# Optimization experiments

Hardware: AMD Instinct MI355X
Metric: run time of the kernel (lower is better)

## Reference

```python
import jax, jax.numpy as jnp
import numpy as np
import math

D_MODEL = 128
N_HEAD = 8
D_K = D_MODEL // N_HEAD
NEG_INF = -1e30


def setup_inputs() -> dict:
    key = jax.random.key(0)
    ks = jax.random.split(key, 8)
    B, N, D = 4, 2048, D_MODEL
    s = 1.0 / math.sqrt(D)
    x = jax.random.normal(ks[0], (B, D, N), dtype=jnp.float32)
    mask = jnp.ones((B, N), dtype=jnp.float32)
    Wq = jax.random.normal(ks[1], (D, D), dtype=jnp.float32) * s
    Wk = jax.random.normal(ks[2], (D, D), dtype=jnp.float32) * s
    Wv = jax.random.normal(ks[3], (D, D), dtype=jnp.float32) * s
    Wfc = jax.random.normal(ks[4], (D, D), dtype=jnp.float32) * s
    z = jnp.zeros((D,), dtype=jnp.float32)
    return {"x": x, "mask": mask, "Wq": Wq, "bq": z, "Wk": Wk, "bk": z,
            "Wv": Wv, "bv": z, "Wfc": Wfc, "bfc": z}


def reference(x, mask, Wq, bq, Wk, bk, Wv, bv, Wfc, bfc):
    # x: [B, D, N], mask: [B, N]
    B, D, N = x.shape
    xt = jnp.swapaxes(x, 1, 2)  # [B, N, D]
    q = (xt @ Wq.T + bq).reshape(B, N, N_HEAD, D_K)
    k = (xt @ Wk.T + bk).reshape(B, N, N_HEAD, D_K)
    v = (xt @ Wv.T + bv).reshape(B, N, N_HEAD, D_K)
    # scores: [B, H, Nq, Nk]; NOTE: original scales by sqrt(d_model), not sqrt(d_k)
    scores = jnp.einsum('bnhd,bmhd->bhnm', q, k) / jnp.sqrt(jnp.float32(D))
    # multiplicative mask_logits over the key dimension
    m = mask[:, None, None, :]  # [B, 1, 1, Nk]
    scores = scores * m + (1.0 - m) * NEG_INF
    atten = jax.nn.softmax(scores, axis=-1)  # dropout is identity (p=0 / eval)
    out = jnp.einsum('bhnm,bmhd->bnhd', atten, v).reshape(B, N, D)
    out = out @ Wfc.T + bfc
    return jnp.swapaxes(out, 1, 2)  # [B, D, N]
```

## Files before the change

### kernel.cpp

```cpp
#include <hip/hip_runtime.h>
#include <stdint.h>

#define BSZ  4
#define NSEQ 2048
#define DM   128
#define NH   8
#define DK   16
#define LOG2E 1.4426950408889634f

typedef __bf16          bf16x8v __attribute__((ext_vector_type(8)));
typedef float           f32x4   __attribute__((ext_vector_type(4)));
typedef float           f32x16  __attribute__((ext_vector_type(16)));
typedef unsigned short  u16x8   __attribute__((ext_vector_type(8)));
typedef unsigned short  u16x4   __attribute__((ext_vector_type(4)));
typedef unsigned int    u32x2   __attribute__((ext_vector_type(2)));

__device__ __forceinline__ unsigned short f2bf(float f) {
    unsigned u = __float_as_uint(f);
    u = (u + 0x7fffu + ((u >> 16) & 1u)) >> 16;
    return (unsigned short)u;
}

__device__ __forceinline__ unsigned int pack2bf(float a, float b) {
#if __has_builtin(__builtin_amdgcn_cvt_pk_bf16_f32)
    typedef __bf16 bf16x2 __attribute__((ext_vector_type(2)));
    bf16x2 v = __builtin_amdgcn_cvt_pk_bf16_f32(a, b);
    return __builtin_bit_cast(unsigned int, v);
#else
    return (unsigned)f2bf(a) | ((unsigned)f2bf(b) << 16);
#endif
}

__device__ __forceinline__ float exp2_(float x) {
#if __has_builtin(__builtin_amdgcn_exp2f)
    return __builtin_amdgcn_exp2f(x);
#else
    return exp2f(x);
#endif
}

__device__ __forceinline__ f32x4 mfma16(u16x8 a, u16x8 b, f32x4 c) {
    return __builtin_amdgcn_mfma_f32_16x16x32_bf16(
        __builtin_bit_cast(bf16x8v, a), __builtin_bit_cast(bf16x8v, b), c, 0, 0, 0);
}
__device__ __forceinline__ f32x16 mfma32(u16x8 a, u16x8 b, f32x16 c) {
    return __builtin_amdgcn_mfma_f32_32x32x16_bf16(
        __builtin_bit_cast(bf16x8v, a), __builtin_bit_cast(bf16x8v, b), c, 0, 0, 0);
}

__global__ __launch_bounds__(256) void k_conv(
    const float* __restrict__ Wq, const float* __restrict__ Wk,
    const float* __restrict__ Wv, const float* __restrict__ Wfc,
    const float* __restrict__ bq, const float* __restrict__ mask,
    unsigned short* __restrict__ WqB, unsigned short* __restrict__ WkB,
    unsigned short* __restrict__ WvB, unsigned short* __restrict__ WfcB,
    float* __restrict__ bqs, float* __restrict__ mbias)
{
    const int t = blockIdx.x * 256 + threadIdx.x;
    const float s = 0.08838834764831845f;
    WqB[t]  = f2bf(Wq[t] * s);
    WkB[t]  = f2bf(Wk[t]);
    WvB[t]  = f2bf(Wv[t]);
    WfcB[t] = f2bf(Wfc[t]);
    if (t < DM) bqs[t] = bq[t] * s;
    if (t < BSZ * NSEQ) mbias[t] = (1.0f - mask[t]) * (-1e30f);
}

__global__ __launch_bounds__(192) void k_qkv(
    const float* __restrict__ x,
    const unsigned short* __restrict__ WqB, const float* __restrict__ bqs,
    const unsigned short* __restrict__ WkB, const float* __restrict__ bk,
    const unsigned short* __restrict__ WvB, const float* __restrict__ bv,
    unsigned short* __restrict__ Q, unsigned short* __restrict__ Kb,
    unsigned short* __restrict__ Vt)
{
    const int lane = threadIdx.x & 63;
    const int mat  = threadIdx.x >> 6;
    const int c    = lane & 15;
    const int quad = lane >> 4;
    const int b    = blockIdx.x >> 7;
    const int n0   = (blockIdx.x & 127) << 4;

    u16x8 xf[4];
#pragma unroll
    for (int kk = 0; kk < 4; ++kk) {
        u16x8 u;
#pragma unroll
        for (int j = 0; j < 8; ++j)
            u[j] = f2bf(x[(b * DM + kk * 32 + quad * 8 + j) * NSEQ + n0 + c]);
        xf[kk] = u;
    }

    const unsigned short* W    = (mat == 0) ? WqB : (mat == 1) ? WkB : WvB;
    const float*          bias = (mat == 0) ? bqs : (mat == 1) ? bk  : bv;

    for (int t = 0; t < 8; ++t) {
        f32x4 acc = {0.f, 0.f, 0.f, 0.f};
#pragma unroll
        for (int kk = 0; kk < 4; ++kk)
            acc = mfma16(*reinterpret_cast<const u16x8*>(
                             W + (t * 16 + c) * DM + kk * 32 + quad * 8),
                         xf[kk], acc);
        if (mat == 2) {
#pragma unroll
            for (int r = 0; r < 4; ++r)
                Vt[((b * NH + t) * DK + quad * 4 + r) * NSEQ + n0 + c] =
                    f2bf(acc[r] + bias[t * 16 + quad * 4 + r]);
        } else {
            u16x4 pk;
#pragma unroll
            for (int r = 0; r < 4; ++r)
                pk[r] = f2bf(acc[r] + bias[t * 16 + quad * 4 + r]);
            *reinterpret_cast<u16x4*>(
                (mat == 0 ? Q : Kb) + ((size_t)(b * NH + t) * NSEQ + n0 + c) * DK +
                quad * 4) = pk;
        }
    }
}

__global__ __launch_bounds__(256, 4) void k_attn(
    const unsigned short* __restrict__ Q,
    const unsigned short* __restrict__ Kb,
    const unsigned short* __restrict__ Vt,
    const float* __restrict__ mbias,
    unsigned short* __restrict__ AO)
{
    __shared__ __align__(16) char smem[19456];
    const int lane = threadIdx.x & 63;
    const int w    = threadIdx.x >> 6;
    const int q32  = lane & 31;
    const int hi   = lane >> 5;
    const int c    = lane & 15;
    const int quad = lane >> 4;

    const int qt   = blockIdx.x * 2 + (w >> 1);
    const int half = w & 1;
    const int b    = qt >> 9;
    const int h    = (qt >> 6) & 7;
    const int n0   = (qt & 63) << 5;
    const int bh   = b * NH + h;

    const u16x8 uq = *reinterpret_cast<const u16x8*>(
        Q + ((size_t)bh * NSEQ + n0 + q32) * DK + 8 * hi);

    const unsigned short* Kp = Kb + (size_t)bh * NSEQ * DK + 8 * hi;
    const unsigned short* Vp = Vt + ((size_t)bh * DK + c) * NSEQ + 8 * quad;
    const float*          mb = mbias + b * NSEQ + 4 * hi;

    char* pbase = smem + w * 2560;
    char* wrow  = pbase + q32 * 80 + 8 * hi;
    const u16x8* rp0 = reinterpret_cast<const u16x8*>(pbase + c * 80 + 16 * quad);
    const u16x8* rp1 = reinterpret_cast<const u16x8*>(pbase + (c + 16) * 80 + 16 * quad);

    float m_run = -1e30f, l_run = 0.f;
    f32x4 o0 = {0.f, 0.f, 0.f, 0.f}, o1 = {0.f, 0.f, 0.f, 0.f};
    const f32x16 z16 = {};

    const int kvbase = half * (NSEQ / 2);
    for (int it = 0; it < 32; ++it) {
        const int kv0 = kvbase + it * 32;
        const u16x8 uk = *reinterpret_cast<const u16x8*>(Kp + (size_t)(kv0 + q32) * DK);
        f32x16 S = mfma32(uk, uq, z16);

        const f32x4 b0 = *reinterpret_cast<const f32x4*>(mb + kv0);
        const f32x4 b1 = *reinterpret_cast<const f32x4*>(mb + kv0 + 8);
        const f32x4 b2 = *reinterpret_cast<const f32x4*>(mb + kv0 + 16);
        const f32x4 b3 = *reinterpret_cast<const f32x4*>(mb + kv0 + 24);
#pragma unroll
        for (int r = 0; r < 4; ++r) {
            S[r]      += b0[r];
            S[4 + r]  += b1[r];
            S[8 + r]  += b2[r];
            S[12 + r] += b3[r];
        }

        float t8[8];
#pragma unroll
        for (int i = 0; i < 8; ++i) t8[i] = fmaxf(S[i], S[i + 8]);
#pragma unroll
        for (int i = 0; i < 4; ++i) t8[i] = fmaxf(t8[i], t8[i + 4]);
        float mx = fmaxf(fmaxf(t8[0], t8[1]), fmaxf(t8[2], t8[3]));
        mx = fmaxf(mx, __shfl_xor(mx, 32, 64));

        const float mn    = fmaxf(m_run, mx);
        const float mnL   = mn * LOG2E;
        const float alpha = exp2_(fmaf(m_run, LOG2E, -mnL));

        float p[16];
#pragma unroll
        for (int i = 0; i < 16; ++i) p[i] = exp2_(fmaf(S[i], LOG2E, -mnL));
        float s8[8];
#pragma unroll
        for (int i = 0; i < 8; ++i) s8[i] = p[i] + p[i + 8];
#pragma unroll
        for (int i = 0; i < 4; ++i) s8[i] = s8[i] + s8[i + 4];
        float ps = (s8[0] + s8[1]) + (s8[2] + s8[3]);
        ps += __shfl_xor(ps, 32, 64);
        l_run = fmaf(l_run, alpha, ps);
        m_run = mn;

        const float a0 = __shfl(alpha, c, 64);
        const float a1 = __shfl(alpha, c + 16, 64);
#pragma unroll
        for (int r = 0; r < 4; ++r) { o0[r] *= a0; o1[r] *= a1; }

        unsigned int pk[8];
#pragma unroll
        for (int s = 0; s < 8; ++s) pk[s] = pack2bf(p[2 * s], p[2 * s + 1]);
#pragma unroll
        for (int g = 0; g < 4; ++g) {
            u32x2 dv = {pk[2 * g], pk[2 * g + 1]};
            *reinterpret_cast<u32x2*>(wrow + 16 * g) = dv;
        }

        const u16x8 up0 = *rp0;
        const u16x8 up1 = *rp1;
        const u16x8 uv  = *reinterpret_cast<const u16x8*>(Vp + kv0);
        o0 = mfma16(uv, up0, o0);
        o1 = mfma16(uv, up1, o1);
    }

    float* stm = reinterpret_cast<float*>(smem + 10240) + w * 64;
    stm[q32]      = m_run;
    stm[32 + q32] = l_run;
    f32x4* ox = reinterpret_cast<f32x4*>(smem + 11264 + w * 2048);
    ox[lane * 2]     = o0;
    ox[lane * 2 + 1] = o1;
    __syncthreads();

    const int pw = w ^ 1;
    const float* stp = reinterpret_cast<const float*>(smem + 10240) + pw * 64;
    const float m2 = stp[q32];
    const float l2 = stp[32 + q32];
    const float mn   = fmaxf(m_run, m2);
    const float f1   = exp2_((m_run - mn) * LOG2E);
    const float f2   = exp2_((m2 - mn) * LOG2E);
    const float inv  = 1.0f / (l_run * f1 + l2 * f2);
    const float s1   = f1 * inv, s2 = f2 * inv;

    const f32x4* oxp = reinterpret_cast<const f32x4*>(smem + 11264 + pw * 2048);
    const f32x4 po0 = oxp[lane * 2];
    const f32x4 po1 = oxp[lane * 2 + 1];

    const float s1a = __shfl(s1, c, 64),      s2a = __shfl(s2, c, 64);
    const float s1b = __shfl(s1, c + 16, 64), s2b = __shfl(s2, c + 16, 64);

    if (half == 0) {
        u16x4 r0, r1;
#pragma unroll
        for (int r = 0; r < 4; ++r) {
            r0[r] = f2bf(o0[r] * s1a + po0[r] * s2a);
            r1[r] = f2bf(o1[r] * s1b + po1[r] * s2b);
        }
        *reinterpret_cast<u16x4*>(
            AO + ((size_t)(b * NSEQ) + n0 + c) * DM + h * DK + quad * 4) = r0;
        *reinterpret_cast<u16x4*>(
            AO + ((size_t)(b * NSEQ) + n0 + 16 + c) * DM + h * DK + quad * 4) = r1;
    }
}

__global__ __launch_bounds__(256) void k_fc(
    const unsigned short* __restrict__ AO,
    const unsigned short* __restrict__ WfcB, const float* __restrict__ bfc,
    float* __restrict__ out)
{
    const int lane = threadIdx.x & 63;
    const int w    = threadIdx.x >> 6;
    const int c    = lane & 15;
    const int quad = lane >> 4;
    const int b    = blockIdx.x >> 7;
    const int n0   = (blockIdx.x & 127) << 4;

    u16x8 af[4];
#pragma unroll
    for (int kk = 0; kk < 4; ++kk)
        af[kk] = *reinterpret_cast<const u16x8*>(
            AO + ((size_t)(b * NSEQ) + n0 + c) * DM + kk * 32 + quad * 8);

#pragma unroll
    for (int tt = 0; tt < 2; ++tt) {
        const int t = w * 2 + tt;
        f32x4 acc = {0.f, 0.f, 0.f, 0.f};
#pragma unroll
        for (int kk = 0; kk < 4; ++kk)
            acc = mfma16(*reinterpret_cast<const u16x8*>(
                             WfcB + (t * 16 + c) * DM + kk * 32 + quad * 8),
                         af[kk], acc);
#pragma unroll
        for (int r = 0; r < 4; ++r)
            out[(size_t)(b * DM + t * 16 + quad * 4 + r) * NSEQ + n0 + c] =
                acc[r] + bfc[t * 16 + quad * 4 + r];
    }
}

extern "C" void kernel_launch(void* const* d_in, const int* in_sizes, int n_in,
                              void* d_out, int out_size, void* d_ws, size_t ws_size,
                              hipStream_t stream)
{
    const float* x    = (const float*)d_in[0];
    const float* mask = (const float*)d_in[1];
    const float* Wq   = (const float*)d_in[2];
    const float* bq   = (const float*)d_in[3];
    const float* Wk   = (const float*)d_in[4];
    const float* bk   = (const float*)d_in[5];
    const float* Wv   = (const float*)d_in[6];
    const float* bv   = (const float*)d_in[7];
    const float* Wfc  = (const float*)d_in[8];
    const float* bfc  = (const float*)d_in[9];
    float* out = (float*)d_out;

    const size_t QKV_ELEMS = (size_t)BSZ * NH * NSEQ * DK;
    unsigned short* Q    = (unsigned short*)d_ws;
    unsigned short* Kb   = Q + QKV_ELEMS;
    unsigned short* Vt   = Kb + QKV_ELEMS;
    unsigned short* AO   = Vt + QKV_ELEMS;
    unsigned short* WqB  = AO + QKV_ELEMS;
    unsigned short* WkB  = WqB + DM * DM;
    unsigned short* WvB  = WkB + DM * DM;
    unsigned short* WfcB = WvB + DM * DM;
    float* bqs   = (float*)(WfcB + DM * DM);
    float* mbias = bqs + DM;

    k_conv<<<64, 256, 0, stream>>>(Wq, Wk, Wv, Wfc, bq, mask,
                                   WqB, WkB, WvB, WfcB, bqs, mbias);
    k_qkv<<<512, 192, 0, stream>>>(x, WqB, bqs, WkB, bk, WvB, bv, Q, Kb, Vt);
    k_attn<<<1024, 256, 0, stream>>>(Q, Kb, Vt, mbias, AO);
    k_fc<<<512, 256, 0, stream>>>(AO, WfcB, bfc, out);
}
```

Baseline: 136.7 us.

## Split attention KV across four waves, fold log2e into scale, double grids

Each attention block now handles one 32-query tile, and its four waves each cover a quarter of the KV sequence. Each wave processes 64 keys per iteration, and the four partial results are merged in shared memory through a cooperative reduction. The log2e factor is folded into the Q weight scale and the mask bias, which removes the per-element FMAs before exp2. The QKV and FC kernels are split across twice as many blocks to raise parallelism. The cost is larger shared memory use and more blocks with less work each, which adds launch and tail overhead.

```diff
diff --git a/kernel.cpp b/kernel.cpp
--- a/kernel.cpp
+++ b/kernel.cpp
@@ -7,6 +7,7 @@
 #define NH   8
 #define DK   16
 #define LOG2E 1.4426950408889634f
+#define SCALE_QL 0.1275156338341935f
 
 typedef __bf16          bf16x8v __attribute__((ext_vector_type(8)));
 typedef float           f32x4   __attribute__((ext_vector_type(4)));
@@ -57,13 +58,12 @@
     float* __restrict__ bqs, float* __restrict__ mbias)
 {
     const int t = blockIdx.x * 256 + threadIdx.x;
-    const float s = 0.08838834764831845f;
-    WqB[t]  = f2bf(Wq[t] * s);
+    WqB[t]  = f2bf(Wq[t] * SCALE_QL);
     WkB[t]  = f2bf(Wk[t]);
     WvB[t]  = f2bf(Wv[t]);
     WfcB[t] = f2bf(Wfc[t]);
-    if (t < DM) bqs[t] = bq[t] * s;
-    if (t < BSZ * NSEQ) mbias[t] = (1.0f - mask[t]) * (-1e30f);
+    if (t < DM) bqs[t] = bq[t] * SCALE_QL;
+    if (t < BSZ * NSEQ) mbias[t] = (1.0f - mask[t]) * (-1e30f * LOG2E);
 }
 
 __global__ __launch_bounds__(192) void k_qkv(
@@ -78,8 +78,9 @@
     const int mat  = threadIdx.x >> 6;
     const int c    = lane & 15;
     const int quad = lane >> 4;
-    const int b    = blockIdx.x >> 7;
-    const int n0   = (blockIdx.x & 127) << 4;
+    const int b    = blockIdx.x >> 8;
+    const int n0   = ((blockIdx.x >> 1) & 127) << 4;
+    const int th   = blockIdx.x & 1;
 
     u16x8 xf[4];
 #pragma unroll
@@ -94,7 +95,9 @@
     const unsigned short* W    = (mat == 0) ? WqB : (mat == 1) ? WkB : WvB;
     const float*          bias = (mat == 0) ? bqs : (mat == 1) ? bk  : bv;
 
-    for (int t = 0; t < 8; ++t) {
+#pragma unroll
+    for (int tt = 0; tt < 4; ++tt) {
+        const int t = th * 4 + tt;
         f32x4 acc = {0.f, 0.f, 0.f, 0.f};
 #pragma unroll
         for (int kk = 0; kk < 4; ++kk)
@@ -122,79 +125,84 @@
     const unsigned short* __restrict__ Q,
     const unsigned short* __restrict__ Kb,
     const unsigned short* __restrict__ Vt,
-    const float* __restrict__ mbias,
+    const float* __restrict__ mb2,
     unsigned short* __restrict__ AO)
 {
-    __shared__ __align__(16) char smem[19456];
-    const int lane = threadIdx.x & 63;
-    const int w    = threadIdx.x >> 6;
+    __shared__ __align__(16) char smem[28672];
+    const int tid  = threadIdx.x;
+    const int lane = tid & 63;
+    const int w    = tid >> 6;
     const int q32  = lane & 31;
     const int hi   = lane >> 5;
     const int c    = lane & 15;
     const int quad = lane >> 4;
 
-    const int qt   = blockIdx.x * 2 + (w >> 1);
-    const int half = w & 1;
-    const int b    = qt >> 9;
-    const int h    = (qt >> 6) & 7;
-    const int n0   = (qt & 63) << 5;
-    const int bh   = b * NH + h;
+    const int b  = blockIdx.x >> 9;
+    const int h  = (blockIdx.x >> 6) & 7;
+    const int n0 = (blockIdx.x & 63) << 5;
+    const int bh = b * NH + h;
 
     const u16x8 uq = *reinterpret_cast<const u16x8*>(
         Q + ((size_t)bh * NSEQ + n0 + q32) * DK + 8 * hi);
 
     const unsigned short* Kp = Kb + (size_t)bh * NSEQ * DK + 8 * hi;
     const unsigned short* Vp = Vt + ((size_t)bh * DK + c) * NSEQ + 8 * quad;
-    const float*          mb = mbias + b * NSEQ + 4 * hi;
-
-    char* pbase = smem + w * 2560;
-    char* wrow  = pbase + q32 * 80 + 8 * hi;
-    const u16x8* rp0 = reinterpret_cast<const u16x8*>(pbase + c * 80 + 16 * quad);
-    const u16x8* rp1 = reinterpret_cast<const u16x8*>(pbase + (c + 16) * 80 + 16 * quad);
+    const float*          mb = mb2 + b * NSEQ + 4 * hi;
+
+    char* pbase = smem + w * 4352;
+    char* wrow  = pbase + q32 * 136 + 8 * hi;
+    const char* rrow0 = pbase + c * 136 + 16 * quad;
+    const char* rrow1 = pbase + (c + 16) * 136 + 16 * quad;
 
     float m_run = -1e30f, l_run = 0.f;
     f32x4 o0 = {0.f, 0.f, 0.f, 0.f}, o1 = {0.f, 0.f, 0.f, 0.f};
     const f32x16 z16 = {};
-
-    const int kvbase = half * (NSEQ / 2);
-    for (int it = 0; it < 32; ++it) {
-        const int kv0 = kvbase + it * 32;
-        const u16x8 uk = *reinterpret_cast<const u16x8*>(Kp + (size_t)(kv0 + q32) * DK);
-        f32x16 S = mfma32(uk, uq, z16);
-
-        const f32x4 b0 = *reinterpret_cast<const f32x4*>(mb + kv0);
-        const f32x4 b1 = *reinterpret_cast<const f32x4*>(mb + kv0 + 8);
-        const f32x4 b2 = *reinterpret_cast<const f32x4*>(mb + kv0 + 16);
-        const f32x4 b3 = *reinterpret_cast<const f32x4*>(mb + kv0 + 24);
-#pragma unroll
-        for (int r = 0; r < 4; ++r) {
-            S[r]      += b0[r];
-            S[4 + r]  += b1[r];
-            S[8 + r]  += b2[r];
-            S[12 + r] += b3[r];
-        }
-
-        float t8[8];
-#pragma unroll
-        for (int i = 0; i < 8; ++i) t8[i] = fmaxf(S[i], S[i + 8]);
-#pragma unroll
-        for (int i = 0; i < 4; ++i) t8[i] = fmaxf(t8[i], t8[i + 4]);
-        float mx = fmaxf(fmaxf(t8[0], t8[1]), fmaxf(t8[2], t8[3]));
+    const int kvb = w * (NSEQ / 4);
+
+    for (int it = 0; it < 8; ++it) {
+        const int kv0 = kvb + it * 64;
+        const u16x8 uk0 = *reinterpret_cast<const u16x8*>(Kp + (size_t)(kv0 + q32) * DK);
+        const u16x8 uk1 = *reinterpret_cast<const u16x8*>(Kp + (size_t)(kv0 + 32 + q32) * DK);
+        f32x16 S0 = mfma32(uk0, uq, z16);
+        f32x16 S1 = mfma32(uk1, uq, z16);
+
+#pragma unroll
+        for (int g = 0; g < 4; ++g) {
+            const f32x4 bg0 = *reinterpret_cast<const f32x4*>(mb + kv0 + 8 * g);
+            const f32x4 bg1 = *reinterpret_cast<const f32x4*>(mb + kv0 + 32 + 8 * g);
+#pragma unroll
+            for (int r = 0; r < 4; ++r) {
+                S0[4 * g + r] += bg0[r];
+                S1[4 * g + r] += bg1[r];
+            }
+        }
+
+        float t16[16];
+#pragma unroll
+        for (int i = 0; i < 16; ++i) t16[i] = fmaxf(S0[i], S1[i]);
+#pragma unroll
+        for (int i = 0; i < 8; ++i) t16[i] = fmaxf(t16[i], t16[i + 8]);
+#pragma unroll
+        for (int i = 0; i < 4; ++i) t16[i] = fmaxf(t16[i], t16[i + 4]);
+        float mx = fmaxf(fmaxf(t16[0], t16[1]), fmaxf(t16[2], t16[3]));
         mx = fmaxf(mx, __shfl_xor(mx, 32, 64));
 
         const float mn    = fmaxf(m_run, mx);
-        const float mnL   = mn * LOG2E;
-        const float alpha = exp2_(fmaf(m_run, LOG2E, -mnL));
-
-        float p[16];
-#pragma unroll
-        for (int i = 0; i < 16; ++i) p[i] = exp2_(fmaf(S[i], LOG2E, -mnL));
-        float s8[8];
-#pragma unroll
-        for (int i = 0; i < 8; ++i) s8[i] = p[i] + p[i + 8];
-#pragma unroll
-        for (int i = 0; i < 4; ++i) s8[i] = s8[i] + s8[i + 4];
-        float ps = (s8[0] + s8[1]) + (s8[2] + s8[3]);
+        const float alpha = exp2_(m_run - mn);
+
+#pragma unroll
+        for (int i = 0; i < 16; ++i) {
+            S0[i] = exp2_(S0[i] - mn);
+            S1[i] = exp2_(S1[i] - mn);
+        }
+        float s16[16];
+#pragma unroll
+        for (int i = 0; i < 16; ++i) s16[i] = S0[i] + S1[i];
+#pragma unroll
+        for (int i = 0; i < 8; ++i) s16[i] += s16[i + 8];
+#pragma unroll
+        for (int i = 0; i < 4; ++i) s16[i] += s16[i + 4];
+        float ps = (s16[0] + s16[1]) + (s16[2] + s16[3]);
         ps += __shfl_xor(ps, 32, 64);
         l_run = fmaf(l_run, alpha, ps);
         m_run = mn;
@@ -204,59 +212,48 @@
 #pragma unroll
         for (int r = 0; r < 4; ++r) { o0[r] *= a0; o1[r] *= a1; }
 
-        unsigned int pk[8];
-#pragma unroll
-        for (int s = 0; s < 8; ++s) pk[s] = pack2bf(p[2 * s], p[2 * s + 1]);
 #pragma unroll
         for (int g = 0; g < 4; ++g) {
-            u32x2 dv = {pk[2 * g], pk[2 * g + 1]};
-            *reinterpret_cast<u32x2*>(wrow + 16 * g) = dv;
-        }
-
-        const u16x8 up0 = *rp0;
-        const u16x8 up1 = *rp1;
-        const u16x8 uv  = *reinterpret_cast<const u16x8*>(Vp + kv0);
-        o0 = mfma16(uv, up0, o0);
-        o1 = mfma16(uv, up1, o1);
+            u32x2 d0 = {pack2bf(S0[4 * g], S0[4 * g + 1]),
+                        pack2bf(S0[4 * g + 2], S0[4 * g + 3])};
+            u32x2 d1 = {pack2bf(S1[4 * g], S1[4 * g + 1]),
+                        pack2bf(S1[4 * g + 2], S1[4 * g + 3])};
+            *reinterpret_cast<u32x2*>(wrow + 16 * g) = d0;
+            *reinterpret_cast<u32x2*>(wrow + 64 + 16 * g) = d1;
+        }
+
+#pragma unroll
+        for (int t = 0; t < 2; ++t) {
+            const u16x8 uv  = *reinterpret_cast<const u16x8*>(Vp + kv0 + 32 * t);
+            const u16x8 up0 = *reinterpret_cast<const u16x8*>(rrow0 + 64 * t);
+            const u16x8 up1 = *reinterpret_cast<const u16x8*>(rrow1 + 64 * t);
+            o0 = mfma16(uv, up0, o0);
+            o1 = mfma16(uv, up1, o1);
+        }
     }
 
-    float* stm = reinterpret_cast<float*>(smem + 10240) + w * 64;
-    stm[q32]      = m_run;
-    stm[32 + q32] = l_run;
-    f32x4* ox = reinterpret_cast<f32x4*>(smem + 11264 + w * 2048);
-    ox[lane * 2]     = o0;
-    ox[lane * 2 + 1] = o1;
+    float* stm = reinterpret_cast<float*>(smem + 17408);
+    float* Osm = reinterpret_cast<float*>(smem + 18432);
+    stm[w * 64 + q32]      = m_run;
+    stm[w * 64 + 32 + q32] = l_run;
+    *reinterpret_cast<f32x4*>(Osm + w * 640 + c * 20 + 4 * quad)        = o0;
+    *reinterpret_cast<f32x4*>(Osm + w * 640 + (c + 16) * 20 + 4 * quad) = o1;
     __syncthreads();
 
-    const int pw = w ^ 1;
-    const float* stp = reinterpret_cast<const float*>(smem + 10240) + pw * 64;
-    const float m2 = stp[q32];
-    const float l2 = stp[32 + q32];
-    const float mn   = fmaxf(m_run, m2);
-    const float f1   = exp2_((m_run - mn) * LOG2E);
-    const float f2   = exp2_((m2 - mn) * LOG2E);
-    const float inv  = 1.0f / (l_run * f1 + l2 * f2);
-    const float s1   = f1 * inv, s2 = f2 * inv;
-
-    const f32x4* oxp = reinterpret_cast<const f32x4*>(smem + 11264 + pw * 2048);
-    const f32x4 po0 = oxp[lane * 2];
-    const f32x4 po1 = oxp[lane * 2 + 1];
-
-    const float s1a = __shfl(s1, c, 64),      s2a = __shfl(s2, c, 64);
-    const float s1b = __shfl(s1, c + 16, 64), s2b = __shfl(s2, c + 16, 64);
-
-    if (half == 0) {
-        u16x4 r0, r1;
-#pragma unroll
-        for (int r = 0; r < 4; ++r) {
-            r0[r] = f2bf(o0[r] * s1a + po0[r] * s2a);
-            r1[r] = f2bf(o1[r] * s1b + po1[r] * s2b);
-        }
-        *reinterpret_cast<u16x4*>(
-            AO + ((size_t)(b * NSEQ) + n0 + c) * DM + h * DK + quad * 4) = r0;
-        *reinterpret_cast<u16x4*>(
-            AO + ((size_t)(b * NSEQ) + n0 + 16 + c) * DM + h * DK + quad * 4) = r1;
-    }
+    const int q   = tid >> 3;
+    const int dk2 = (tid & 7) * 2;
+    const float mA = stm[q],       mB = stm[64 + q];
+    const float mC = stm[128 + q], mD = stm[192 + q];
+    const float mm = fmaxf(fmaxf(mA, mB), fmaxf(mC, mD));
+    const float sA = exp2_(mA - mm), sB = exp2_(mB - mm);
+    const float sC = exp2_(mC - mm), sD = exp2_(mD - mm);
+    const float inv = 1.0f / (stm[32 + q] * sA + stm[96 + q] * sB +
+                              stm[160 + q] * sC + stm[224 + q] * sD);
+    const float* Oq = Osm + q * 20 + dk2;
+    const float v0 = (Oq[0] * sA + Oq[640] * sB + Oq[1280] * sC + Oq[1920] * sD) * inv;
+    const float v1 = (Oq[1] * sA + Oq[641] * sB + Oq[1281] * sC + Oq[1921] * sD) * inv;
+    *reinterpret_cast<unsigned int*>(
+        AO + ((size_t)(b * NSEQ) + n0 + q) * DM + h * DK + dk2) = pack2bf(v0, v1);
 }
 
 __global__ __launch_bounds__(256) void k_fc(
@@ -268,8 +265,9 @@
     const int w    = threadIdx.x >> 6;
     const int c    = lane & 15;
     const int quad = lane >> 4;
-    const int b    = blockIdx.x >> 7;
-    const int n0   = (blockIdx.x & 127) << 4;
+    const int b    = blockIdx.x >> 8;
+    const int n0   = ((blockIdx.x >> 1) & 127) << 4;
+    const int t    = (blockIdx.x & 1) * 4 + w;
 
     u16x8 af[4];
 #pragma unroll
@@ -277,20 +275,16 @@
         af[kk] = *reinterpret_cast<const u16x8*>(
             AO + ((size_t)(b * NSEQ) + n0 + c) * DM + kk * 32 + quad * 8);
 
-#pragma unroll
-    for (int tt = 0; tt < 2; ++tt) {
-        const int t = w * 2 + tt;
-        f32x4 acc = {0.f, 0.f, 0.f, 0.f};
-#pragma unroll
-        for (int kk = 0; kk < 4; ++kk)
-            acc = mfma16(*reinterpret_cast<const u16x8*>(
-                             WfcB + (t * 16 + c) * DM + kk * 32 + quad * 8),
-                         af[kk], acc);
-#pragma unroll
-        for (int r = 0; r < 4; ++r)
-            out[(size_t)(b * DM + t * 16 + quad * 4 + r) * NSEQ + n0 + c] =
-                acc[r] + bfc[t * 16 + quad * 4 + r];
-    }
+    f32x4 acc = {0.f, 0.f, 0.f, 0.f};
+#pragma unroll
+    for (int kk = 0; kk < 4; ++kk)
+        acc = mfma16(*reinterpret_cast<const u16x8*>(
+                         WfcB + (t * 16 + c) * DM + kk * 32 + quad * 8),
+                     af[kk], acc);
+#pragma unroll
+    for (int r = 0; r < 4; ++r)
+        out[(size_t)(b * DM + t * 16 + quad * 4 + r) * NSEQ + n0 + c] =
+            acc[r] + bfc[t * 16 + quad * 4 + r];
 }
 
 extern "C" void kernel_launch(void* const* d_in, const int* in_sizes, int n_in,
@@ -323,7 +317,7 @@
 
     k_conv<<<64, 256, 0, stream>>>(Wq, Wk, Wv, Wfc, bq, mask,
                                    WqB, WkB, WvB, WfcB, bqs, mbias);
-    k_qkv<<<512, 192, 0, stream>>>(x, WqB, bqs, WkB, bk, WvB, bv, Q, Kb, Vt);
-    k_attn<<<1024, 256, 0, stream>>>(Q, Kb, Vt, mbias, AO);
-    k_fc<<<512, 256, 0, stream>>>(AO, WfcB, bfc, out);
-}
+    k_qkv<<<1024, 192, 0, stream>>>(x, WqB, bqs, WkB, bk, WvB, bv, Q, Kb, Vt);
+    k_attn<<<2048, 256, 0, stream>>>(Q, Kb, Vt, mbias, AO);
+    k_fc<<<1024, 256, 0, stream>>>(AO, WfcB, bfc, out);
+}
```

Result: no change. 136.1 us (-0.4%).
